# Optimization experiments

Hardware: AMD Instinct MI355X
Metric: run time of the kernel (lower is better)

## Reference

```python
import jax, jax.numpy as jnp
import numpy as np
from jax import lax

B, S, E, H, V, L = 16, 256, 256, 256, 50000, 9


def setup_inputs() -> dict:
    key = jax.random.key(0)
    ks = jax.random.split(key, 12)
    s = 0.05
    return {
        "input_ids": jax.random.randint(ks[0], (B, S), 0, V),
        "attention_mask": jnp.ones((B, S), dtype=jnp.int32),
        "labels": jax.random.randint(ks[1], (B, S), 0, L),
        "embedding": jax.random.normal(ks[2], (V, E), jnp.float32) * s,
        "w_ih_l0": jax.random.normal(ks[3], (2, 4 * H, E), jnp.float32) * s,
        "w_ih_rest": jax.random.normal(ks[4], (3, 2, 4 * H, 2 * H), jnp.float32) * s,
        "w_hh": jax.random.normal(ks[5], (4, 2, 4 * H, H), jnp.float32) * s,
        "b": jax.random.normal(ks[6], (4, 2, 2, 4 * H), jnp.float32) * s,
        "ln_g": jnp.ones((2 * H,), jnp.float32),
        "ln_b": jnp.zeros((2 * H,), jnp.float32),
        "lin_w": jax.random.normal(ks[7], (L, 2 * H), jnp.float32) * s,
        "lin_b": jnp.zeros((L,), jnp.float32),
        "crf_start": jax.random.normal(ks[8], (L,), jnp.float32) * s,
        "crf_end": jax.random.normal(ks[9], (L,), jnp.float32) * s,
        "crf_trans": jax.random.normal(ks[10], (L, L), jnp.float32) * s,
    }


def _lstm_dir(x, w_ih, w_hh, b_ih, b_hh, reverse):
    # x: [B,S,in]; PyTorch gate order i,f,g,o packed along 4H.
    Bb = x.shape[0]
    Hh = w_hh.shape[1]
    xg = jnp.einsum('bsi,gi->bsg', x, w_ih) + b_ih + b_hh  # precompute input projection
    if reverse:
        xg = xg[:, ::-1]

    def step(carry, g):
        h, c = carry
        g = g + h @ w_hh.T
        i, f, gg, o = jnp.split(g, 4, axis=-1)
        c = jax.nn.sigmoid(f) * c + jax.nn.sigmoid(i) * jnp.tanh(gg)
        h = jax.nn.sigmoid(o) * jnp.tanh(c)
        return (h, c), h

    z = jnp.zeros((Bb, Hh), x.dtype)
    _, hs = lax.scan(step, (z, z), jnp.swapaxes(xg, 0, 1))
    hs = jnp.swapaxes(hs, 0, 1)  # [B,S,H]
    if reverse:
        hs = hs[:, ::-1]
    return hs


def _forward(input_ids, attention_mask, labels, embedding, w_ih_l0, w_ih_rest,
             w_hh, b, ln_g, ln_b, lin_w, lin_b, crf_start, crf_end, crf_trans):
    x = embedding[input_ids]  # [B,S,E]
    for layer in range(4):
        wf = w_ih_l0[0] if layer == 0 else w_ih_rest[layer - 1, 0]
        wb = w_ih_l0[1] if layer == 0 else w_ih_rest[layer - 1, 1]
        hf = _lstm_dir(x, wf, w_hh[layer, 0], b[layer, 0, 0], b[layer, 0, 1], False)
        hb = _lstm_dir(x, wb, w_hh[layer, 1], b[layer, 1, 0], b[layer, 1, 1], True)
        x = jnp.concatenate([hf, hb], axis=-1)  # [B,S,2H]
    # dropout is identity in eval mode
    mu = x.mean(-1, keepdims=True)
    var = ((x - mu) ** 2).mean(-1, keepdims=True)
    x = (x - mu) * lax.rsqrt(var + 1e-5) * ln_g + ln_b
    logits = jnp.einsum('bsh,lh->bsl', x, lin_w) + lin_b  # emissions [B,S,L]

    # CRF negative log-likelihood (torchcrf semantics, reduction='sum')
    Bb = logits.shape[0]
    mask_f = attention_mask.astype(logits.dtype)
    bidx = jnp.arange(Bb)
    first = labels[:, 0]
    num = crf_start[first] + logits[bidx, 0, first]
    em_t = jnp.swapaxes(logits, 0, 1)[1:]  # [S-1,B,L]
    tprev = labels[:, :-1].T
    tcur = labels[:, 1:].T
    mt = mask_f[:, 1:].T

    def num_step(s, inp):
        e, tp, tc, m = inp
        return s + (crf_trans[tp, tc] + e[bidx, tc]) * m, None

    num, _ = lax.scan(num_step, num, (em_t, tprev, tcur, mt))
    last = jnp.sum(attention_mask, axis=1).astype(jnp.int32) - 1
    num = num + crf_end[labels[bidx, last]]

    alpha = crf_start + logits[:, 0]  # [B,L]

    def den_step(a, inp):
        e, m = inp
        nxt = jax.nn.logsumexp(a[:, :, None] + crf_trans[None] + e[:, None, :], axis=1)
        return jnp.where(m[:, None] > 0, nxt, a), None

    alpha, _ = lax.scan(den_step, alpha, (em_t, mt))
    denom = jax.nn.logsumexp(alpha + crf_end, axis=-1)
    loss = -(num - denom).sum()
    return logits, loss


def reference(input_ids, attention_mask, labels, embedding, w_ih_l0, w_ih_rest,
              w_hh, b, ln_g, ln_b, lin_w, lin_b, crf_start, crf_end, crf_trans):
    return _forward(input_ids, attention_mask, labels, embedding, w_ih_l0,
                    w_ih_rest, w_hh, b, ln_g, ln_b, lin_w, lin_b,
                    crf_start, crf_end, crf_trans)
```

## Files before the change

kernel.cpp:

```cpp
#include <hip/hip_runtime.h>
#include <math.h>
#include <stdint.h>

#define BB 16
#define SS 256
#define LL 9
#define ROWS 4096
#define HP 272

typedef __attribute__((ext_vector_type(8))) short short8;
typedef __attribute__((ext_vector_type(4))) float f32x4;
typedef __attribute__((ext_vector_type(8))) int i32x8;

#define HSCALE 256.0f
#define LOG2E  1.44269504f
#define WCONST 1477.3199f
#define SCALE_ONE 0x7F7F7F7Fu
#define SCALE_IFO 0x6D6D6D6Du
#define SCALE_G   0x6E6E6E6Eu

__device__ __forceinline__ unsigned short f2bf(float f) {
  unsigned u = __float_as_uint(f);
  return (unsigned short)((u + 0x7FFF + ((u >> 16) & 1)) >> 16);
}
__device__ __forceinline__ float bf2f(unsigned short s) {
  return __uint_as_float(((unsigned)s) << 16);
}

__device__ __forceinline__ void gl2lds16(const void* g, void* l) {
  __builtin_amdgcn_global_load_lds(
      (const __attribute__((address_space(1))) void*)g,
      (__attribute__((address_space(3))) void*)l, 16, 0, 0);
}

__global__ __launch_bounds__(256) void embed_bf16(
    const int* __restrict__ ids, const float* __restrict__ emb,
    unsigned short* __restrict__ x0) {
  int row = blockIdx.x;
  int id = ids[row];
  x0[(size_t)row * 256 + threadIdx.x] = f2bf(emb[(size_t)id * 256 + threadIdx.x]);
}

__global__ __launch_bounds__(64) void pack_whh_mx(
    const float* __restrict__ w, unsigned* __restrict__ wfrag) {
  int nb = blockIdx.x, ks2 = blockIdx.y, z = blockIdx.z;
  int lane = threadIdx.x, qq = lane >> 4, col = lane & 15;
  int g = nb >> 4;
  float csc = (g == 2) ? WCONST : -WCONST;
  const float* wp = w + (size_t)z * 1024 * 256 + (size_t)(nb * 16 + col) * 256 +
                    ks2 * 128 + qq * 32;
  unsigned* op = wfrag + (((size_t)(z * 64 + nb) * 2 + ks2) * 64 + lane) * 8;
#pragma unroll
  for (int u = 0; u < 8; ++u) {
    float v0 = wp[u * 4 + 0] * csc, v1 = wp[u * 4 + 1] * csc;
    float v2 = wp[u * 4 + 2] * csc, v3 = wp[u * 4 + 3] * csc;
    unsigned pk = __builtin_amdgcn_cvt_pk_fp8_f32(v0, v1, 0, false);
    pk = __builtin_amdgcn_cvt_pk_fp8_f32(v2, v3, pk, true);
    op[u] = pk;
  }
}

__global__ __launch_bounds__(256) void bias_perm(
    const float* __restrict__ b2, float* __restrict__ biasPF) {
  int i = blockIdx.x * 256 + threadIdx.x;
  int l = i >> 11, r = i & 2047;
  int dir = r >> 10, np = r & 1023;
  int n = ((np & 3) << 8) + (np >> 2);
  float cg = ((np & 3) == 2) ? (2.0f * LOG2E) : (-LOG2E);
  biasPF[i] = (b2[l * 4096 + dir * 2048 + n] + b2[l * 4096 + dir * 2048 + 1024 + n]) * cg;
}

__global__ __launch_bounds__(256) void prep_wih(
    const float* __restrict__ w_l0, const float* __restrict__ w_rest,
    unsigned short* __restrict__ wp, const long* __restrict__ woff_dummy) {
  int l = blockIdx.z;
  int Ksh = l ? 9 : 8;
  int K = 1 << Ksh;
  long total = (long)2 * 1024 * K;
  long idx = (long)blockIdx.x * 256 + threadIdx.x;
  if (idx >= total) return;
  int k = (int)(idx & (K - 1));
  long r = idx >> Ksh;
  int np = (int)(r & 1023), dir = (int)(r >> 10);
  int nph = ((np & 3) << 8) + (np >> 2);
  float cg = ((np & 3) == 2) ? (2.0f * LOG2E) : (-LOG2E);
  const float* src = l ? (w_rest + (size_t)(l - 1) * 2 * 1024 * 512) : w_l0;
  size_t off = l ? (524288 + (size_t)(l - 1) * 1048576) : 0;
  wp[off + idx] = f2bf(src[((size_t)dir * 1024 + nph) * K + k] * cg);
}

__global__ __launch_bounds__(512) void gemm_xg128(
    const unsigned short* __restrict__ A, int K,
    const unsigned short* __restrict__ BP,
    const float* __restrict__ biasPF,
    unsigned short* __restrict__ xgP) {
  int dir = blockIdx.z;
  int n0 = blockIdx.x * 128, m0 = blockIdx.y * 128;
  int tid = threadIdx.x;
  int wv = tid >> 6, lane = tid & 63, quad = lane >> 4, col = lane & 15;
  __shared__ unsigned short As[128 * 32];
  __shared__ unsigned short Bs[128 * 32];
  const unsigned short* Bw = BP + (size_t)dir * 1024 * K;

  int srow = lane >> 2;
  int scol = (lane & 3) * 8;
  const unsigned short* ga = A + (size_t)(m0 + wv * 16 + srow) * K + scol;
  const unsigned short* gb = Bw + (size_t)(n0 + wv * 16 + srow) * K + scol;
  unsigned short* lA = &As[wv * 512];
  unsigned short* lB = &Bs[wv * 512];

  int wm = wv & 1;
  int wn = wv >> 1;
  f32x4 acc[4][2];
#pragma unroll
  for (int mt = 0; mt < 4; ++mt)
#pragma unroll
    for (int nt = 0; nt < 2; ++nt) acc[mt][nt] = (f32x4){0.f, 0.f, 0.f, 0.f};

  for (int k0 = 0; k0 < K; k0 += 32) {
    __syncthreads();
    gl2lds16(ga, lA);
    gl2lds16(gb, lB);
    ga += 32; gb += 32;
    __syncthreads();
    short8 bf0 = *(const short8*)&Bs[(wn * 32 + col) * 32 + quad * 8];
    short8 bf1 = *(const short8*)&Bs[(wn * 32 + 16 + col) * 32 + quad * 8];
#pragma unroll
    for (int mt = 0; mt < 4; ++mt) {
      short8 af = *(const short8*)&As[(wm * 64 + mt * 16 + col) * 32 + quad * 8];
      acc[mt][0] = __builtin_amdgcn_mfma_f32_16x16x32_bf16(af, bf0, acc[mt][0], 0, 0, 0);
      acc[mt][1] = __builtin_amdgcn_mfma_f32_16x16x32_bf16(af, bf1, acc[mt][1], 0, 0, 0);
    }
  }

#pragma unroll
  for (int nt = 0; nt < 2; ++nt) {
    int np = n0 + wn * 32 + nt * 16 + col;
    float bia = biasPF[dir * 1024 + np];
#pragma unroll
    for (int mt = 0; mt < 4; ++mt) {
#pragma unroll
      for (int r = 0; r < 4; ++r) {
        int row = m0 + wm * 64 + mt * 16 + quad * 4 + r;
        xgP[((size_t)dir * ROWS + row) * 1024 + np] = f2bf(acc[mt][nt][r] + bia);
      }
    }
  }
}

__global__ __launch_bounds__(512, 2) void lstm_mx(
    const unsigned short* __restrict__ xgP,
    const unsigned* __restrict__ wfrag,
    unsigned short* __restrict__ xout) {
  int dir = blockIdx.x & 1;
  int bg = blockIdx.x >> 1;
  int tid = threadIdx.x;
  int wv = tid >> 6, lane = tid & 63;
  int quad = lane >> 4, col = lane & 15;

  __shared__ __align__(16) unsigned char Hfrag[2][2 * HP];

  {
    int* hz = (int*)&Hfrag[0][0];
    for (int i = tid; i < HP; i += 512) hz[i] = 0;
  }

  i32x8 wf[2][4][2];
#pragma unroll
  for (int hbi = 0; hbi < 2; ++hbi)
#pragma unroll
    for (int g = 0; g < 4; ++g) {
      int nb = g * 16 + 2 * wv + hbi;
#pragma unroll
      for (int ks2 = 0; ks2 < 2; ++ks2)
        wf[hbi][g][ks2] = *(const i32x8*)(wfrag +
            (((size_t)(dir * 64 + nb) * 2 + ks2) * 64 + lane) * 8);
    }

  int aoff = ((lane & 15) >> 3) * HP + (lane >> 4) * 32;

  int hbsel = quad & 1;
  int bq = quad >> 1;
  int j = 32 * wv + 16 * hbsel + col;
  int b = bg * 2 + bq;
  int pos0 = dir ? (SS - 1) : 0;
  int dstep = dir ? -1 : 1;
  const unsigned short* xq_ptr =
      xgP + ((size_t)dir * ROWS + (size_t)b * SS + pos0) * 1024 + j * 4;
  unsigned short* xo_ptr = xout + ((size_t)b * SS + pos0) * 512 + dir * 256 + j;
  int xq_d = dstep * 1024;
  int xo_d = dstep * 512;
  int hw = bq * HP + j;

  float Cp = 0.f;
  unsigned short ph = 0;
  unsigned short* xo_prev = xo_ptr;
  int cur = 0;
  __syncthreads();

  for (int t = 0; t < SS; ++t) {
    if (t) *xo_prev = ph;
    ushort4 xq = *(const ushort4*)xq_ptr;
    xq_ptr += xq_d;

    i32x8 af0 = *(const i32x8*)&Hfrag[cur][aoff];
    i32x8 af1 = *(const i32x8*)&Hfrag[cur][aoff + 128];
    f32x4 acc[2][4];
#pragma unroll
    for (int hbi = 0; hbi < 2; ++hbi) {
#pragma unroll
      for (int g = 0; g < 4; ++g) {
        f32x4 a = (f32x4){0.f, 0.f, 0.f, 0.f};
        a = __builtin_amdgcn_mfma_scale_f32_16x16x128_f8f6f4(
                af0, wf[hbi][g][0], a, 0, 0, 0, SCALE_ONE, 0,
                (g == 2) ? SCALE_G : SCALE_IFO);
        a = __builtin_amdgcn_mfma_scale_f32_16x16x128_f8f6f4(
                af1, wf[hbi][g][1], a, 0, 0, 0, SCALE_ONE, 0,
                (g == 2) ? SCALE_G : SCALE_IFO);
        acc[hbi][g] = a;
      }
    }

    int nxt = cur ^ 1;
    float a_i = hbsel ? acc[1][0][0] : acc[0][0][0];
    float a_f = hbsel ? acc[1][1][0] : acc[0][1][0];
    float a_g = hbsel ? acc[1][2][0] : acc[0][2][0];
    float a_o = hbsel ? acc[1][3][0] : acc[0][3][0];
    float gi = a_i + bf2f(xq.x);
    float gf = a_f + bf2f(xq.y);
    float gt = a_g + bf2f(xq.z);
    float go = a_o + bf2f(xq.w);
    float si = __builtin_amdgcn_rcpf(1.0f + __builtin_amdgcn_exp2f(gi));
    float sf = __builtin_amdgcn_rcpf(1.0f + __builtin_amdgcn_exp2f(gf));
    float so = __builtin_amdgcn_rcpf(1.0f + __builtin_amdgcn_exp2f(go));
    float rg = __builtin_amdgcn_rcpf(1.0f + __builtin_amdgcn_exp2f(gt));
    float tg2 = fmaf(-4.0f * LOG2E, rg, 2.0f * LOG2E);
    Cp = fmaf(sf, Cp, si * tg2);
    float rc = __builtin_amdgcn_rcpf(1.0f + __builtin_amdgcn_exp2f(Cp));
    float h = so * fmaf(-2.0f, rc, 1.0f);
    unsigned pk = __builtin_amdgcn_cvt_pk_fp8_f32(h * HSCALE, h * HSCALE, 0, false);
    Hfrag[nxt][hw] = (unsigned char)(pk & 0xFF);
    ph = f2bf(h);
    xo_prev = xo_ptr;
    xo_ptr += xo_d;
    __syncthreads();
    cur = nxt;
  }
  *xo_prev = ph;
}

__global__ __launch_bounds__(64) void ln_logits(
    const unsigned short* __restrict__ X, const float* __restrict__ g,
    const float* __restrict__ bt, const float* __restrict__ W,
    const float* __restrict__ lb, float* __restrict__ out) {
  int row = blockIdx.x;
  int lane = threadIdx.x;
  const unsigned short* x = X + (size_t)row * 512;
  float v[8];
  float s = 0.f, s2 = 0.f;
#pragma unroll
  for (int i = 0; i < 8; ++i) {
    v[i] = bf2f(x[lane + 64 * i]);
    s += v[i];
    s2 += v[i] * v[i];
  }
#pragma unroll
  for (int off = 32; off; off >>= 1) {
    s += __shfl_down(s, off, 64);
    s2 += __shfl_down(s2, off, 64);
  }
  s = __shfl(s, 0, 64);
  s2 = __shfl(s2, 0, 64);
  float mu = s * (1.f / 512.f);
  float var = s2 * (1.f / 512.f) - mu * mu;
  float rstd = rsqrtf(var + 1e-5f);
  float y[8];
#pragma unroll
  for (int i = 0; i < 8; ++i) {
    int e = lane + 64 * i;
    y[i] = (v[i] - mu) * rstd * g[e] + bt[e];
  }
  for (int l = 0; l < LL; ++l) {
    float p = 0.f;
#pragma unroll
    for (int i = 0; i < 8; ++i) p += y[i] * W[(size_t)l * 512 + lane + 64 * i];
#pragma unroll
    for (int off = 32; off; off >>= 1) p += __shfl_down(p, off, 64);
    if (lane == 0) out[(size_t)row * LL + l] = p + lb[l];
  }
}

__global__ __launch_bounds__(256) void crf_kernel(
    const float* __restrict__ logits, const int* __restrict__ labels,
    const int* __restrict__ mask, const float* __restrict__ cs,
    const float* __restrict__ ce, const float* __restrict__ ct,
    float* __restrict__ loss_out) {
  __shared__ float trans[9][12];
  __shared__ float alpha[2][BB][12];
  __shared__ float numsh[BB];
  __shared__ float res[BB];
  int tid = threadIdx.x;
  int b = tid >> 4;
  int i = tid & 15;
  if (tid < 81) trans[tid / 9][tid % 9] = ct[tid];
  __syncthreads();
  const float* lg = logits + (size_t)b * SS * LL;
  const int* lbp = labels + (size_t)b * SS;
  const int* mk = mask + (size_t)b * SS;

  float np = 0.f;
  int msum = 0;
  for (int t = i; t < SS; t += 16) {
    msum += mk[t];
    if (t == 0) {
      int l0 = lbp[0];
      np += cs[l0] + lg[l0];
    } else {
      float m = (float)mk[t];
      np += (trans[lbp[t - 1]][lbp[t]] + lg[(size_t)t * LL + lbp[t]]) * m;
    }
  }
#pragma unroll
  for (int off = 8; off; off >>= 1) {
    np += __shfl_down(np, off, 16);
    msum += __shfl_down(msum, off, 16);
  }
  if (i == 0) {
    int last = msum - 1;
    numsh[b] = np + ce[lbp[last]];
  }

  if (i < LL) alpha[0][b][i] = cs[i] + lg[i];
  int cur = 0;
  for (int t = 1; t < SS; ++t) {
    if (i < LL) {
      float e = lg[(size_t)t * LL + i];
      float av[9];
      float mmax = -1e30f;
#pragma unroll
      for (int p = 0; p < LL; ++p) {
        float vv = alpha[cur][b][p] + trans[p][i];
        av[p] = vv;
        mmax = fmaxf(mmax, vv);
      }
      float ssum = 0.f;
#pragma unroll
      for (int p = 0; p < LL; ++p) ssum += __expf(av[p] - mmax);
      float anew = e + mmax + logf(ssum);
      float aold = alpha[cur][b][i];
      alpha[cur ^ 1][b][i] = (mk[t] > 0) ? anew : aold;
    }
    cur ^= 1;
  }
  if (i == 0) {
    float arr[9];
    float m2 = -1e30f;
#pragma unroll
    for (int cc = 0; cc < LL; ++cc) {
      arr[cc] = alpha[cur][b][cc] + ce[cc];
      m2 = fmaxf(m2, arr[cc]);
    }
    float ssd = 0.f;
#pragma unroll
    for (int cc = 0; cc < LL; ++cc) ssd += __expf(arr[cc] - m2);
    float denom = m2 + logf(ssd);
    res[b] = numsh[b] - denom;
  }
  __syncthreads();
  if (tid == 0) {
    float Lsum = 0.f;
    for (int b2 = 0; b2 < BB; ++b2) Lsum += res[b2];
    loss_out[0] = -Lsum;
  }
}

extern "C" void kernel_launch(void* const* d_in, const int* in_sizes, int n_in,
                              void* d_out, int out_size, void* d_ws, size_t ws_size,
                              hipStream_t stream) {
  const int* input_ids = (const int*)d_in[0];
  const int* attn_mask = (const int*)d_in[1];
  const int* labels = (const int*)d_in[2];
  const float* embedding = (const float*)d_in[3];
  const float* w_ih_l0 = (const float*)d_in[4];
  const float* w_ih_rest = (const float*)d_in[5];
  const float* w_hh = (const float*)d_in[6];
  const float* bvec = (const float*)d_in[7];
  const float* ln_g = (const float*)d_in[8];
  const float* ln_b = (const float*)d_in[9];
  const float* lin_w = (const float*)d_in[10];
  const float* lin_b = (const float*)d_in[11];
  const float* crf_start = (const float*)d_in[12];
  const float* crf_end = (const float*)d_in[13];
  const float* crf_trans = (const float*)d_in[14];
  float* out = (float*)d_out;
  char* base = (char*)d_ws;

  unsigned short* x0    = (unsigned short*)(base);
  unsigned short* xoutA = (unsigned short*)(base + (2u << 20));
  unsigned short* xoutB = (unsigned short*)(base + (6u << 20));
  unsigned short* xgP   = (unsigned short*)(base + (10u << 20));
  unsigned*       wfrag = (unsigned*)(base + (26u << 20));
  float*          biasPF= (float*)(base + (28u << 20));
  unsigned short* wihP  = (unsigned short*)(base + (29u << 20));

  embed_bf16<<<ROWS, 256, 0, stream>>>(input_ids, embedding, x0);
  pack_whh_mx<<<dim3(64, 2, 8), 64, 0, stream>>>(w_hh, wfrag);
  bias_perm<<<32, 256, 0, stream>>>(bvec, biasPF);
  prep_wih<<<dim3(4096, 1, 4), 256, 0, stream>>>(w_ih_l0, w_ih_rest, wihP, nullptr);

  const size_t WOFF[4] = {0, 524288, 1572864, 2621440};

  const unsigned short* cur = x0;
  unsigned short* nxt = xoutA;
  for (int l = 0; l < 4; ++l) {
    int K = l ? 512 : 256;
    gemm_xg128<<<dim3(8, 32, 2), 512, 0, stream>>>(
        cur, K, wihP + WOFF[l], biasPF + (size_t)l * 2048, xgP);
    lstm_mx<<<16, 512, 0, stream>>>(xgP, wfrag + (size_t)l * 131072, nxt);
    cur = nxt;
    nxt = (nxt == xoutA) ? xoutB : xoutA;
  }

  ln_logits<<<ROWS, 64, 0, stream>>>(cur, ln_g, ln_b, lin_w, lin_b, out);
  crf_kernel<<<1, 256, 0, stream>>>(out, labels, attn_mask, crf_start, crf_end,
                                    crf_trans, out + (size_t)ROWS * LL);
}
```

Before: 1.198 ms.

## Pre-pack W_ih into MFMA fragments and double-buffer GEMM A tiles

prep_wih now writes the input-projection weights directly in MFMA B-fragment order, so the GEMM loads B straight from global memory into registers instead of staging it through LDS. The GEMM drops to 256 threads with a 4x4 accumulator tile per wave, double-buffers a padded LDS A tile, and prefetches the next k-chunk into registers. Separately, the LSTM step seeds the MFMA accumulator with the precomputed input gate value, which removes the post-MFMA adds from the serial recurrence. The cost is more registers per thread and fewer waves per GEMM block.

Measured after the change: 1.207 ms. No clear change (+0.7%).

```diff
diff --git a/kernel.cpp b/kernel.cpp
--- a/kernel.cpp
+++ b/kernel.cpp
@@ -7,6 +7,7 @@
 #define LL 9
 #define ROWS 4096
 #define HP 272
+#define AP 40
 
 typedef __attribute__((ext_vector_type(8))) short short8;
 typedef __attribute__((ext_vector_type(4))) float f32x4;
@@ -25,12 +26,6 @@
 }
 __device__ __forceinline__ float bf2f(unsigned short s) {
   return __uint_as_float(((unsigned)s) << 16);
-}
-
-__device__ __forceinline__ void gl2lds16(const void* g, void* l) {
-  __builtin_amdgcn_global_load_lds(
-      (const __attribute__((address_space(1))) void*)g,
-      (__attribute__((address_space(3))) void*)l, 16, 0, 0);
 }
 
 __global__ __launch_bounds__(256) void embed_bf16(
@@ -72,16 +67,23 @@
 
 __global__ __launch_bounds__(256) void prep_wih(
     const float* __restrict__ w_l0, const float* __restrict__ w_rest,
-    unsigned short* __restrict__ wp, const long* __restrict__ woff_dummy) {
+    unsigned short* __restrict__ wp) {
   int l = blockIdx.z;
-  int Ksh = l ? 9 : 8;
-  int K = 1 << Ksh;
+  int K = l ? 512 : 256;
+  int kcb = l ? 4 : 3;
   long total = (long)2 * 1024 * K;
   long idx = (long)blockIdx.x * 256 + threadIdx.x;
   if (idx >= total) return;
-  int k = (int)(idx & (K - 1));
-  long r = idx >> Ksh;
-  int np = (int)(r & 1023), dir = (int)(r >> 10);
+  int j = (int)(idx & 7);
+  long r = idx >> 3;
+  int lane = (int)(r & 63); r >>= 6;
+  int kc = (int)(r & ((1 << kcb) - 1));
+  long r2 = r >> kcb;
+  int ntile = (int)(r2 & 63);
+  int dir = (int)(r2 >> 6);
+  int quad = lane >> 4, col = lane & 15;
+  int np = ntile * 16 + col;
+  int k = kc * 32 + quad * 8 + j;
   int nph = ((np & 3) << 8) + (np >> 2);
   float cg = ((np & 3) == 2) ? (2.0f * LOG2E) : (-LOG2E);
   const float* src = l ? (w_rest + (size_t)(l - 1) * 2 * 1024 * 512) : w_l0;
@@ -89,53 +91,78 @@
   wp[off + idx] = f2bf(src[((size_t)dir * 1024 + nph) * K + k] * cg);
 }
 
-__global__ __launch_bounds__(512) void gemm_xg128(
+__global__ __launch_bounds__(256) void gemm_xg_bfrag(
     const unsigned short* __restrict__ A, int K,
-    const unsigned short* __restrict__ BP,
+    const unsigned short* __restrict__ Bfrag,
     const float* __restrict__ biasPF,
     unsigned short* __restrict__ xgP) {
   int dir = blockIdx.z;
   int n0 = blockIdx.x * 128, m0 = blockIdx.y * 128;
   int tid = threadIdx.x;
   int wv = tid >> 6, lane = tid & 63, quad = lane >> 4, col = lane & 15;
-  __shared__ unsigned short As[128 * 32];
-  __shared__ unsigned short Bs[128 * 32];
-  const unsigned short* Bw = BP + (size_t)dir * 1024 * K;
-
-  int srow = lane >> 2;
-  int scol = (lane & 3) * 8;
-  const unsigned short* ga = A + (size_t)(m0 + wv * 16 + srow) * K + scol;
-  const unsigned short* gb = Bw + (size_t)(n0 + wv * 16 + srow) * K + scol;
-  unsigned short* lA = &As[wv * 512];
-  unsigned short* lB = &Bs[wv * 512];
-
-  int wm = wv & 1;
-  int wn = wv >> 1;
-  f32x4 acc[4][2];
+  int wm = wv & 1, wn = wv >> 1;
+  __shared__ unsigned short As[2][128 * AP];
+
+  int KC = K >> 5;
+  const unsigned short* Bf = Bfrag + (size_t)dir * 64 * KC * 512;
+  const unsigned short* bfp[4];
+#pragma unroll
+  for (int nt = 0; nt < 4; ++nt)
+    bfp[nt] = Bf + (((size_t)((n0 >> 4) + wn * 4 + nt) * KC) * 64 + lane) * 8;
+
+  int srow = tid >> 1;
+  int scol = (tid & 1) * 16;
+  const unsigned short* ga = A + (size_t)(m0 + srow) * K + scol;
+  int woff = srow * AP + scol;
+
+  f32x4 acc[4][4];
 #pragma unroll
   for (int mt = 0; mt < 4; ++mt)
 #pragma unroll
-    for (int nt = 0; nt < 2; ++nt) acc[mt][nt] = (f32x4){0.f, 0.f, 0.f, 0.f};
-
-  for (int k0 = 0; k0 < K; k0 += 32) {
+    for (int nt = 0; nt < 4; ++nt) acc[mt][nt] = (f32x4){0.f, 0.f, 0.f, 0.f};
+
+  short8 a0 = *(const short8*)ga;
+  short8 a1 = *(const short8*)(ga + 8);
+  short8 bcur[4];
+#pragma unroll
+  for (int nt = 0; nt < 4; ++nt) bcur[nt] = *(const short8*)bfp[nt];
+  *(short8*)&As[0][woff] = a0;
+  *(short8*)&As[0][woff + 8] = a1;
+  __syncthreads();
+
+  int cur = 0;
+  for (int kc = 0; kc < KC; ++kc) {
+    bool more = (kc + 1) < KC;
+    short8 na0, na1, bnext[4];
+    if (more) {
+      na0 = *(const short8*)(ga + (kc + 1) * 32);
+      na1 = *(const short8*)(ga + (kc + 1) * 32 + 8);
+#pragma unroll
+      for (int nt = 0; nt < 4; ++nt)
+        bnext[nt] = *(const short8*)(bfp[nt] + (size_t)(kc + 1) * 512);
+    }
+    short8 af[4];
+#pragma unroll
+    for (int mt = 0; mt < 4; ++mt)
+      af[mt] = *(const short8*)&As[cur][(wm * 64 + mt * 16 + col) * AP + quad * 8];
+#pragma unroll
+    for (int mt = 0; mt < 4; ++mt)
+#pragma unroll
+      for (int nt = 0; nt < 4; ++nt)
+        acc[mt][nt] = __builtin_amdgcn_mfma_f32_16x16x32_bf16(af[mt], bcur[nt], acc[mt][nt], 0, 0, 0);
+    if (more) {
+      *(short8*)&As[cur ^ 1][woff] = na0;
+      *(short8*)&As[cur ^ 1][woff + 8] = na1;
+#pragma unroll
+      for (int nt = 0; nt < 4; ++nt) bcur[nt] = bnext[nt];
+    }
     __syncthreads();
-    gl2lds16(ga, lA);
-    gl2lds16(gb, lB);
-    ga += 32; gb += 32;
-    __syncthreads();
-    short8 bf0 = *(const short8*)&Bs[(wn * 32 + col) * 32 + quad * 8];
-    short8 bf1 = *(const short8*)&Bs[(wn * 32 + 16 + col) * 32 + quad * 8];
-#pragma unroll
-    for (int mt = 0; mt < 4; ++mt) {
-      short8 af = *(const short8*)&As[(wm * 64 + mt * 16 + col) * 32 + quad * 8];
-      acc[mt][0] = __builtin_amdgcn_mfma_f32_16x16x32_bf16(af, bf0, acc[mt][0], 0, 0, 0);
-      acc[mt][1] = __builtin_amdgcn_mfma_f32_16x16x32_bf16(af, bf1, acc[mt][1], 0, 0, 0);
-    }
-  }
-
-#pragma unroll
-  for (int nt = 0; nt < 2; ++nt) {
-    int np = n0 + wn * 32 + nt * 16 + col;
+    cur ^= 1;
+  }
+
+#pragma unroll
+  for (int nt = 0; nt < 4; ++nt) {
+    int np = n0 + wn * 64 + nt * 16 + col;
     float bia = biasPF[dir * 1024 + np];
 #pragma unroll
     for (int mt = 0; mt < 4; ++mt) {
@@ -202,6 +229,7 @@
     if (t) *xo_prev = ph;
     ushort4 xq = *(const ushort4*)xq_ptr;
     xq_ptr += xq_d;
+    float xg4[4] = {bf2f(xq.x), bf2f(xq.y), bf2f(xq.z), bf2f(xq.w)};
 
     i32x8 af0 = *(const i32x8*)&Hfrag[cur][aoff];
     i32x8 af1 = *(const i32x8*)&Hfrag[cur][aoff + 128];
@@ -210,7 +238,7 @@
     for (int hbi = 0; hbi < 2; ++hbi) {
 #pragma unroll
       for (int g = 0; g < 4; ++g) {
-        f32x4 a = (f32x4){0.f, 0.f, 0.f, 0.f};
+        f32x4 a = (f32x4){xg4[g], 0.f, 0.f, 0.f};
         a = __builtin_amdgcn_mfma_scale_f32_16x16x128_f8f6f4(
                 af0, wf[hbi][g][0], a, 0, 0, 0, SCALE_ONE, 0,
                 (g == 2) ? SCALE_G : SCALE_IFO);
@@ -222,14 +250,10 @@
     }
 
     int nxt = cur ^ 1;
-    float a_i = hbsel ? acc[1][0][0] : acc[0][0][0];
-    float a_f = hbsel ? acc[1][1][0] : acc[0][1][0];
-    float a_g = hbsel ? acc[1][2][0] : acc[0][2][0];
-    float a_o = hbsel ? acc[1][3][0] : acc[0][3][0];
-    float gi = a_i + bf2f(xq.x);
-    float gf = a_f + bf2f(xq.y);
-    float gt = a_g + bf2f(xq.z);
-    float go = a_o + bf2f(xq.w);
+    float gi = hbsel ? acc[1][0][0] : acc[0][0][0];
+    float gf = hbsel ? acc[1][1][0] : acc[0][1][0];
+    float gt = hbsel ? acc[1][2][0] : acc[0][2][0];
+    float go = hbsel ? acc[1][3][0] : acc[0][3][0];
     float si = __builtin_amdgcn_rcpf(1.0f + __builtin_amdgcn_exp2f(gi));
     float sf = __builtin_amdgcn_rcpf(1.0f + __builtin_amdgcn_exp2f(gf));
     float so = __builtin_amdgcn_rcpf(1.0f + __builtin_amdgcn_exp2f(go));
@@ -406,7 +430,7 @@
   embed_bf16<<<ROWS, 256, 0, stream>>>(input_ids, embedding, x0);
   pack_whh_mx<<<dim3(64, 2, 8), 64, 0, stream>>>(w_hh, wfrag);
   bias_perm<<<32, 256, 0, stream>>>(bvec, biasPF);
-  prep_wih<<<dim3(4096, 1, 4), 256, 0, stream>>>(w_ih_l0, w_ih_rest, wihP, nullptr);
+  prep_wih<<<dim3(4096, 1, 4), 256, 0, stream>>>(w_ih_l0, w_ih_rest, wihP);
 
   const size_t WOFF[4] = {0, 524288, 1572864, 2621440};
 
@@ -414,7 +438,7 @@
   unsigned short* nxt = xoutA;
   for (int l = 0; l < 4; ++l) {
     int K = l ? 512 : 256;
-    gemm_xg128<<<dim3(8, 32, 2), 512, 0, stream>>>(
+    gemm_xg_bfrag<<<dim3(8, 32, 2), 256, 0, stream>>>(
         cur, K, wihP + WOFF[l], biasPF + (size_t)l * 2048, xgP);
     lstm_mx<<<16, 512, 0, stream>>>(xgP, wfrag + (size_t)l * 131072, nxt);
     cur = nxt;
```
